# Kernel tuning notes

Measured on AMD Instinct MI355X. Metric: run time of the kernel, lower is better.

## Reference

```python
import jax, jax.numpy as jnp
import numpy as np

NUM_HEADS = 16
ATT_DIM = 1024
DEPTH = ATT_DIM // NUM_HEADS
LN_EPS = 1e-3  # keras LayerNormalization() default (hparams epsilon not passed through)


def setup_inputs() -> dict:
    key = jax.random.key(0)
    ks = jax.random.split(key, 16)
    B, S, D = 2, 2048, ATT_DIM
    s = 1.0 / np.sqrt(D)
    return {
        "query": jax.random.normal(ks[0], (B, S, D), jnp.float32),
        "key": jax.random.normal(ks[1], (B, S, D), jnp.float32),
        "value": jax.random.normal(ks[2], (B, S, D), jnp.float32),
        "Wq": jax.random.normal(ks[3], (D, ATT_DIM), jnp.float32) * s,
        "bq": jnp.zeros((ATT_DIM,), jnp.float32),
        "Wk": jax.random.normal(ks[4], (D, ATT_DIM), jnp.float32) * s,
        "bk": jnp.zeros((ATT_DIM,), jnp.float32),
        "Wv": jax.random.normal(ks[5], (D, ATT_DIM), jnp.float32) * s,
        "bv": jnp.zeros((ATT_DIM,), jnp.float32),
        "Wo": jax.random.normal(ks[6], (ATT_DIM, ATT_DIM), jnp.float32) * s,
        "bo": jnp.zeros((ATT_DIM,), jnp.float32),
        "gamma": jnp.ones((ATT_DIM,), jnp.float32),
        "beta": jnp.zeros((ATT_DIM,), jnp.float32),
    }


def _split_heads(x, B):
    # [B, S, D] -> [B, H, S, depth]
    return x.reshape(B, -1, NUM_HEADS, DEPTH).transpose(0, 2, 1, 3)


def reference(query, key, value, Wq, bq, Wk, bk, Wv, bv, Wo, bo, gamma, beta):
    B = query.shape[0]
    q = _split_heads(query @ Wq + bq, B)  # [B,H,Sq,d]
    k = _split_heads(key @ Wk + bk, B)    # [B,H,Sk,d]
    v = _split_heads(value @ Wv + bv, B)  # [B,H,Sk,d]
    scale = 1.0 / jnp.sqrt(jnp.asarray(DEPTH, q.dtype))
    logits = jnp.einsum('bhqd,bhkd->bhqk', q, k) * scale  # [B,H,Sq,Sk]
    attn = jax.nn.softmax(logits, axis=-1)
    ctx = jnp.einsum('bhqk,bhkd->bhqd', attn, v)  # [B,H,Sq,d]
    out = ctx.transpose(0, 2, 1, 3).reshape(B, -1, ATT_DIM)  # [B,Sq,D]
    out = out @ Wo + bo
    # LayerNorm over last dim (keras default epsilon=1e-3)
    mu = jnp.mean(out, axis=-1, keepdims=True)
    var = jnp.var(out, axis=-1, keepdims=True)
    out = (out - mu) * jax.lax.rsqrt(var + LN_EPS) * gamma + beta
    return out, attn
```

## Files before the change

### kernel.cpp

```cpp
#include <hip/hip_runtime.h>
#include <cstdint>
#include <cstddef>


#define S_LEN 2048
#define D_MODEL 1024
#define N_HEADS 16
#define DEPTH 64
#define BATCH 2
#define OUT0_ELEMS (BATCH * S_LEN * D_MODEL)

typedef __attribute__((ext_vector_type(8))) short short8;
typedef __attribute__((ext_vector_type(4))) short short4v;
typedef __attribute__((ext_vector_type(4))) float float4v;
typedef __attribute__((ext_vector_type(4))) uint16_t u16x4;

__device__ __forceinline__ float bf2f(uint16_t h) {
    uint32_t u = ((uint32_t)h) << 16;
    return __builtin_bit_cast(float, u);
}
__device__ __forceinline__ uint16_t f2bf(float f) {
    uint32_t u = __builtin_bit_cast(uint32_t, f);
    u += 0x7fffu + ((u >> 16) & 1u);
    return (uint16_t)(u >> 16);
}

__device__ __forceinline__ void async_load16(const void* g, void* l) {
    __builtin_amdgcn_global_load_lds(
        (const __attribute__((address_space(1))) void*)g,
        (__attribute__((address_space(3))) void*)l, 16, 0, 0);
}

template <typename Epi>
__device__ __forceinline__ void gemm_core_128x128(
    const uint16_t* __restrict__ A, const uint16_t* __restrict__ Bt,
    int K, Epi&& epi)
{
    __shared__ __align__(16) uint16_t la[128 * 32];
    __shared__ __align__(16) uint16_t lb[128 * 32];
    const int t = threadIdx.x;
    const int wave = t >> 6, lane = t & 63;
    const int quad = lane >> 4, lr = lane & 15;
    const int wm = (wave & 1) * 64, wn = (wave >> 1) * 64;
    const int row_a = t >> 2;
    const int kk = (t & 3) * 8;

    float4v acc[4][4] = {};

    for (int k0 = 0; k0 < K; k0 += 32) {
        async_load16(A  + (row_a      ) * K + k0 + kk, (char*)la + t * 16);
        async_load16(A  + (row_a + 64 ) * K + k0 + kk, (char*)la + 4096 + t * 16);
        async_load16(Bt + (row_a      ) * K + k0 + kk, (char*)lb + t * 16);
        async_load16(Bt + (row_a + 64 ) * K + k0 + kk, (char*)lb + 4096 + t * 16);
        __syncthreads();

        short8 af[4], bfr[4];
        #pragma unroll
        for (int i = 0; i < 4; i++)
            af[i] = *(const short8*)&la[(wm + i * 16 + lr) * 32 + quad * 8];
        #pragma unroll
        for (int j = 0; j < 4; j++)
            bfr[j] = *(const short8*)&lb[(wn + j * 16 + lr) * 32 + quad * 8];
        #pragma unroll
        for (int i = 0; i < 4; i++)
            #pragma unroll
            for (int j = 0; j < 4; j++)
                acc[i][j] = __builtin_amdgcn_mfma_f32_16x16x32_bf16(
                    af[i], bfr[j], acc[i][j], 0, 0, 0);
        __syncthreads();
    }

    #pragma unroll
    for (int i = 0; i < 4; i++)
        #pragma unroll
        for (int j = 0; j < 4; j++)
            #pragma unroll
            for (int r = 0; r < 4; r++)
                epi(wm + i * 16 + quad * 4 + r, wn + j * 16 + lr, acc[i][j][r]);
}

template <typename Epi>
__device__ __forceinline__ void gemm_split_128x128(
    const uint16_t* __restrict__ Ah, const uint16_t* __restrict__ Al,
    const uint16_t* __restrict__ Bh, const uint16_t* __restrict__ Bl,
    int K, Epi&& epi)
{
    __shared__ __align__(16) uint16_t lah[128 * 32];
    __shared__ __align__(16) uint16_t lal[128 * 32];
    __shared__ __align__(16) uint16_t lbh[128 * 32];
    __shared__ __align__(16) uint16_t lbl[128 * 32];
    const int t = threadIdx.x;
    const int wave = t >> 6, lane = t & 63;
    const int quad = lane >> 4, lr = lane & 15;
    const int wm = (wave & 1) * 64, wn = (wave >> 1) * 64;
    const int row_a = t >> 2;
    const int kk = (t & 3) * 8;

    float4v acc[4][4] = {};

    for (int k0 = 0; k0 < K; k0 += 32) {
        async_load16(Ah + (row_a     ) * K + k0 + kk, (char*)lah + t * 16);
        async_load16(Ah + (row_a + 64) * K + k0 + kk, (char*)lah + 4096 + t * 16);
        async_load16(Al + (row_a     ) * K + k0 + kk, (char*)lal + t * 16);
        async_load16(Al + (row_a + 64) * K + k0 + kk, (char*)lal + 4096 + t * 16);
        async_load16(Bh + (row_a     ) * K + k0 + kk, (char*)lbh + t * 16);
        async_load16(Bh + (row_a + 64) * K + k0 + kk, (char*)lbh + 4096 + t * 16);
        async_load16(Bl + (row_a     ) * K + k0 + kk, (char*)lbl + t * 16);
        async_load16(Bl + (row_a + 64) * K + k0 + kk, (char*)lbl + 4096 + t * 16);
        __syncthreads();

        short8 fah[4], fal[4], fbh[4], fbl[4];
        #pragma unroll
        for (int i = 0; i < 4; i++) {
            int off = (wm + i * 16 + lr) * 32 + quad * 8;
            fah[i] = *(const short8*)&lah[off];
            fal[i] = *(const short8*)&lal[off];
        }
        #pragma unroll
        for (int j = 0; j < 4; j++) {
            int off = (wn + j * 16 + lr) * 32 + quad * 8;
            fbh[j] = *(const short8*)&lbh[off];
            fbl[j] = *(const short8*)&lbl[off];
        }
        #pragma unroll
        for (int i = 0; i < 4; i++)
            #pragma unroll
            for (int j = 0; j < 4; j++) {
                acc[i][j] = __builtin_amdgcn_mfma_f32_16x16x32_bf16(
                    fah[i], fbh[j], acc[i][j], 0, 0, 0);
                acc[i][j] = __builtin_amdgcn_mfma_f32_16x16x32_bf16(
                    fah[i], fbl[j], acc[i][j], 0, 0, 0);
                acc[i][j] = __builtin_amdgcn_mfma_f32_16x16x32_bf16(
                    fal[i], fbh[j], acc[i][j], 0, 0, 0);
            }
        __syncthreads();
    }

    #pragma unroll
    for (int i = 0; i < 4; i++)
        #pragma unroll
        for (int j = 0; j < 4; j++)
            #pragma unroll
            for (int r = 0; r < 4; r++)
                epi(wm + i * 16 + quad * 4 + r, wn + j * 16 + lr, acc[i][j][r]);
}


__global__ __launch_bounds__(256) void prep_w_kernel(
    const float* __restrict__ wq, const float* __restrict__ wk,
    const float* __restrict__ wv, const float* __restrict__ wo,
    uint16_t* __restrict__ wqh, uint16_t* __restrict__ wql,
    uint16_t* __restrict__ wkh, uint16_t* __restrict__ wkl,
    uint16_t* __restrict__ wvt, uint16_t* __restrict__ wot)
{
    const int z = blockIdx.z;
    const float* src = z == 0 ? wq : z == 1 ? wk : z == 2 ? wv : wo;
    int idx = blockIdx.x * 256 + threadIdx.x;
    int n = idx >> 10, k = idx & 1023;
    float v = src[k * D_MODEL + n];
    uint16_t hi = f2bf(v);
    if (z == 0) { wqh[idx] = hi; wql[idx] = f2bf(v - bf2f(hi)); }
    else if (z == 1) { wkh[idx] = hi; wkl[idx] = f2bf(v - bf2f(hi)); }
    else if (z == 2) { wvt[idx] = hi; }
    else { wot[idx] = hi; }
}

__global__ __launch_bounds__(256) void split_x_kernel(
    const float* __restrict__ q, const float* __restrict__ k,
    const float* __restrict__ v,
    uint16_t* __restrict__ xqh, uint16_t* __restrict__ xql,
    uint16_t* __restrict__ xkh, uint16_t* __restrict__ xkl,
    uint16_t* __restrict__ xv)
{
    const int z = blockIdx.z;
    const float* src = z == 0 ? q : z == 1 ? k : v;
    int idx = (blockIdx.x * 256 + threadIdx.x) * 4;
    float4v f = *(const float4v*)(src + idx);
    u16x4 hi, lo;
    #pragma unroll
    for (int e = 0; e < 4; e++) {
        hi[e] = f2bf(f[e]);
        lo[e] = f2bf(f[e] - bf2f(hi[e]));
    }
    if (z == 0) { *(u16x4*)(xqh + idx) = hi; *(u16x4*)(xql + idx) = lo; }
    else if (z == 1) { *(u16x4*)(xkh + idx) = hi; *(u16x4*)(xkl + idx) = lo; }
    else { *(u16x4*)(xv + idx) = hi; }
}


__global__ __launch_bounds__(256) void qkproj_kernel(
    const uint16_t* __restrict__ xqh, const uint16_t* __restrict__ xql,
    const uint16_t* __restrict__ xkh, const uint16_t* __restrict__ xkl,
    const uint16_t* __restrict__ wqh, const uint16_t* __restrict__ wql,
    const uint16_t* __restrict__ wkh, const uint16_t* __restrict__ wkl,
    const float* __restrict__ bq, const float* __restrict__ bk,
    uint16_t* __restrict__ qh, uint16_t* __restrict__ ql,
    uint16_t* __restrict__ kh, uint16_t* __restrict__ kl)
{
    const int z = blockIdx.z;
    const uint16_t* Ah = (z == 0 ? xqh : xkh) + (size_t)blockIdx.y * 128 * D_MODEL;
    const uint16_t* Al = (z == 0 ? xql : xkl) + (size_t)blockIdx.y * 128 * D_MODEL;
    const uint16_t* Bh = (z == 0 ? wqh : wkh) + (size_t)blockIdx.x * 128 * D_MODEL;
    const uint16_t* Bl = (z == 0 ? wql : wkl) + (size_t)blockIdx.x * 128 * D_MODEL;
    const float* bias = z == 0 ? bq : bk;
    uint16_t* oh = z == 0 ? qh : kh;
    uint16_t* ol = z == 0 ? ql : kl;
    const int m0 = blockIdx.y * 128, n0 = blockIdx.x * 128;

    gemm_split_128x128(Ah, Al, Bh, Bl, D_MODEL, [&](int r, int c, float v) {
        int m = m0 + r, n = n0 + c;
        float val = v + bias[n];
        int b = m >> 11, s2 = m & 2047;
        int h = n >> 6, dp = n & 63;
        size_t o = (((size_t)(b * N_HEADS + h)) * S_LEN + s2) * DEPTH + dp;
        uint16_t hi = f2bf(val);
        oh[o] = hi;
        ol[o] = f2bf(val - bf2f(hi));
    });
}

__global__ __launch_bounds__(256) void vproj_kernel(
    const uint16_t* __restrict__ xv, const uint16_t* __restrict__ wvt,
    const float* __restrict__ bv, uint16_t* __restrict__ vt)
{
    const uint16_t* A  = xv + (size_t)blockIdx.y * 128 * D_MODEL;
    const uint16_t* Bt = wvt + (size_t)blockIdx.x * 128 * D_MODEL;
    const int m0 = blockIdx.y * 128, n0 = blockIdx.x * 128;

    gemm_core_128x128(A, Bt, D_MODEL, [&](int r, int c, float v) {
        int m = m0 + r, n = n0 + c;
        int b = m >> 11, s2 = m & 2047;
        int h = n >> 6, dp = n & 63;
        vt[(((size_t)(b * N_HEADS + h)) * DEPTH + dp) * S_LEN + s2] = f2bf(v + bv[n]);
    });
}

__global__ __launch_bounds__(512, 4) void attn_fused_kernel(
    const uint16_t* __restrict__ qh, const uint16_t* __restrict__ ql,
    const uint16_t* __restrict__ kh, const uint16_t* __restrict__ kl,
    const uint16_t* __restrict__ vt,
    float* __restrict__ attn, uint16_t* __restrict__ ctx)
{
    __shared__ __align__(16) uint16_t lkh[128 * 64];
    __shared__ __align__(16) uint16_t lkl[128 * 64];
    __shared__ __align__(16) uint16_t lvt[64 * 128];

    const int bh = blockIdx.y;
    const int b = bh >> 4, h = bh & 15;
    const int m0 = blockIdx.x * 128;
    const int t = threadIdx.x;
    const int wave = t >> 6, lane = t & 63;
    const int quad = lane >> 4, lr = lane & 15;
    const int q0 = m0 + wave * 16;
    const int mask = (lr & 7) << 4;

    const size_t qoff = ((size_t)bh * S_LEN + q0 + lr) * DEPTH + quad * 8;
    const short8 fqh0 = *(const short8*)&qh[qoff];
    const short8 fqh1 = *(const short8*)&qh[qoff + 32];
    const short8 fql0 = *(const short8*)&ql[qoff];
    const short8 fql1 = *(const short8*)&ql[qoff + 32];

    const uint16_t* khd = kh + (size_t)bh * S_LEN * DEPTH;
    const uint16_t* kld = kl + (size_t)bh * S_LEN * DEPTH;
    const uint16_t* vhd = vt + (size_t)bh * DEPTH * S_LEN;
    const int o1 = t * 16, o2 = 8192 + t * 16;
    const int kr1 = o1 >> 7, ke1 = ((o1 & 127) ^ ((kr1 & 7) << 4)) >> 1;
    const int kr2 = o2 >> 7, ke2 = ((o2 & 127) ^ ((kr2 & 7) << 4)) >> 1;
    const int vr1 = o1 >> 8, ve1 = ((o1 & 255) ^ ((vr1 & 7) << 4)) >> 1;
    const int vr2 = o2 >> 8, ve2 = ((o2 & 255) ^ ((vr2 & 7) << 4)) >> 1;

    float4v cacc[4] = {};
    float sum = 0.f;

    for (int kc = 0; kc < S_LEN; kc += 128) {
        async_load16(khd + (size_t)(kc + kr1) * DEPTH + ke1, (char*)lkh + o1);
        async_load16(khd + (size_t)(kc + kr2) * DEPTH + ke2, (char*)lkh + o2);
        async_load16(kld + (size_t)(kc + kr1) * DEPTH + ke1, (char*)lkl + o1);
        async_load16(kld + (size_t)(kc + kr2) * DEPTH + ke2, (char*)lkl + o2);
        async_load16(vhd + (size_t)vr1 * S_LEN + kc + ve1, (char*)lvt + o1);
        async_load16(vhd + (size_t)vr2 * S_LEN + kc + ve2, (char*)lvt + o2);
        __syncthreads();

        #pragma unroll
        for (int nt = 0; nt < 8; ++nt) {
            const int rowb = (nt * 16 + lr) * 128;
            const int cb0 = (quad * 16) ^ mask;
            short8 ah0 = *(const short8*)((const char*)lkh + rowb + cb0);
            short8 ah1 = *(const short8*)((const char*)lkh + rowb + (cb0 ^ 64));
            short8 al0 = *(const short8*)((const char*)lkl + rowb + cb0);
            short8 al1 = *(const short8*)((const char*)lkl + rowb + (cb0 ^ 64));
            float4v a = {0.f, 0.f, 0.f, 0.f};
            a = __builtin_amdgcn_mfma_f32_16x16x32_bf16(ah0, fqh0, a, 0, 0, 0);
            a = __builtin_amdgcn_mfma_f32_16x16x32_bf16(ah1, fqh1, a, 0, 0, 0);
            a = __builtin_amdgcn_mfma_f32_16x16x32_bf16(al0, fqh0, a, 0, 0, 0);
            a = __builtin_amdgcn_mfma_f32_16x16x32_bf16(al1, fqh1, a, 0, 0, 0);
            a = __builtin_amdgcn_mfma_f32_16x16x32_bf16(ah0, fql0, a, 0, 0, 0);
            a = __builtin_amdgcn_mfma_f32_16x16x32_bf16(ah1, fql1, a, 0, 0, 0);

            short4v pa;
            #pragma unroll
            for (int r = 0; r < 4; ++r) {
                float e = __expf(a[r] * 0.125f);
                sum += e;
                pa[r] = (short)f2bf(e);
            }
            #pragma unroll
            for (int dt = 0; dt < 4; ++dt) {
                const int vb = (dt * 16 + lr) * 256
                             + ((nt * 32 + quad * 8) ^ mask);
                short4v bv = *(const short4v*)((const char*)lvt + vb);
                cacc[dt] = __builtin_amdgcn_mfma_f32_16x16x16bf16_1k(
                    pa, bv, cacc[dt], 0, 0, 0);
            }
        }
        __syncthreads();
    }

    sum += __shfl_xor(sum, 16);
    sum += __shfl_xor(sum, 32);
    const float inv = 1.0f / sum;

    #pragma unroll
    for (int r = 0; r < 4; ++r) {
        const float invr = __shfl(inv, quad * 4 + r);
        #pragma unroll
        for (int dt = 0; dt < 4; ++dt) {
            ctx[((size_t)(b * S_LEN + q0 + quad * 4 + r)) * D_MODEL
                + h * DEPTH + dt * 16 + lr] = f2bf(cacc[dt][r] * invr);
        }
    }

    float* arow = attn + (size_t)bh * S_LEN * S_LEN + (size_t)(q0 + lr) * S_LEN;
    for (int kc = 0; kc < S_LEN; kc += 128) {
        async_load16(khd + (size_t)(kc + kr1) * DEPTH + ke1, (char*)lkh + o1);
        async_load16(khd + (size_t)(kc + kr2) * DEPTH + ke2, (char*)lkh + o2);
        async_load16(kld + (size_t)(kc + kr1) * DEPTH + ke1, (char*)lkl + o1);
        async_load16(kld + (size_t)(kc + kr2) * DEPTH + ke2, (char*)lkl + o2);
        __syncthreads();

        #pragma unroll
        for (int nt = 0; nt < 8; ++nt) {
            const int rowb = (nt * 16 + lr) * 128;
            const int cb0 = (quad * 16) ^ mask;
            short8 ah0 = *(const short8*)((const char*)lkh + rowb + cb0);
            short8 ah1 = *(const short8*)((const char*)lkh + rowb + (cb0 ^ 64));
            short8 al0 = *(const short8*)((const char*)lkl + rowb + cb0);
            short8 al1 = *(const short8*)((const char*)lkl + rowb + (cb0 ^ 64));
            float4v a = {0.f, 0.f, 0.f, 0.f};
            a = __builtin_amdgcn_mfma_f32_16x16x32_bf16(ah0, fqh0, a, 0, 0, 0);
            a = __builtin_amdgcn_mfma_f32_16x16x32_bf16(ah1, fqh1, a, 0, 0, 0);
            a = __builtin_amdgcn_mfma_f32_16x16x32_bf16(al0, fqh0, a, 0, 0, 0);
            a = __builtin_amdgcn_mfma_f32_16x16x32_bf16(al1, fqh1, a, 0, 0, 0);
            a = __builtin_amdgcn_mfma_f32_16x16x32_bf16(ah0, fql0, a, 0, 0, 0);
            a = __builtin_amdgcn_mfma_f32_16x16x32_bf16(ah1, fql1, a, 0, 0, 0);

            float4v p;
            #pragma unroll
            for (int r = 0; r < 4; ++r)
                p[r] = __expf(a[r] * 0.125f) * inv;
            *(float4v*)&arow[kc + nt * 16 + quad * 4] = p;
        }
        __syncthreads();
    }
}

__global__ __launch_bounds__(256) void proj_kernel(
    const uint16_t* __restrict__ ctx, const uint16_t* __restrict__ wot,
    const float* __restrict__ bo, float* __restrict__ pre)
{
    const uint16_t* A  = ctx + (size_t)blockIdx.y * 128 * D_MODEL;
    const uint16_t* Bt = wot + (size_t)blockIdx.x * 128 * D_MODEL;
    const int m0 = blockIdx.y * 128, n0 = blockIdx.x * 128;

    gemm_core_128x128(A, Bt, D_MODEL, [&](int r, int c, float v) {
        pre[(size_t)(m0 + r) * D_MODEL + (n0 + c)] = v + bo[n0 + c];
    });
}

__global__ __launch_bounds__(256) void ln_kernel(
    const float* __restrict__ pre, const float* __restrict__ gamma,
    const float* __restrict__ beta, float* __restrict__ out)
{
    const int t = threadIdx.x;
    const int row = blockIdx.x;
    const float4v x = *(const float4v*)(pre + (size_t)row * D_MODEL + t * 4);
    float s  = x[0] + x[1] + x[2] + x[3];
    float ss = x[0]*x[0] + x[1]*x[1] + x[2]*x[2] + x[3]*x[3];
    #pragma unroll
    for (int off = 32; off > 0; off >>= 1) {
        s  += __shfl_xor(s, off);
        ss += __shfl_xor(ss, off);
    }
    __shared__ float red[8];
    const int wave = t >> 6, lane = t & 63;
    if (lane == 0) { red[wave] = s; red[4 + wave] = ss; }
    __syncthreads();
    s  = (red[0] + red[1]) + (red[2] + red[3]);
    ss = (red[4] + red[5]) + (red[6] + red[7]);
    float mu  = s * (1.0f / 1024.0f);
    float var = ss * (1.0f / 1024.0f) - mu * mu;
    float inv = rsqrtf(var + 1e-3f);

    float4v g = *(const float4v*)(gamma + t * 4);
    float4v bb = *(const float4v*)(beta + t * 4);
    float4v o;
    #pragma unroll
    for (int j = 0; j < 4; j++)
        o[j] = (x[j] - mu) * inv * g[j] + bb[j];
    *(float4v*)(out + (size_t)row * D_MODEL + t * 4) = o;
}


extern "C" void kernel_launch(void* const* d_in, const int* in_sizes, int n_in,
                              void* d_out, int out_size, void* d_ws, size_t ws_size,
                              hipStream_t stream)
{
    const float* q_in = (const float*)d_in[0];
    const float* k_in = (const float*)d_in[1];
    const float* v_in = (const float*)d_in[2];
    const float* Wq   = (const float*)d_in[3];
    const float* bq   = (const float*)d_in[4];
    const float* Wk   = (const float*)d_in[5];
    const float* bk   = (const float*)d_in[6];
    const float* Wv   = (const float*)d_in[7];
    const float* bv   = (const float*)d_in[8];
    const float* Wo   = (const float*)d_in[9];
    const float* bo   = (const float*)d_in[10];
    const float* gamma= (const float*)d_in[11];
    const float* beta = (const float*)d_in[12];

    char* ws = (char*)d_ws;
    uint16_t* wqh = (uint16_t*)(ws);
    uint16_t* wql = (uint16_t*)(ws + (2u  << 20));
    uint16_t* wkh = (uint16_t*)(ws + (4u  << 20));
    uint16_t* wkl = (uint16_t*)(ws + (6u  << 20));
    uint16_t* wvt = (uint16_t*)(ws + (8u  << 20));
    uint16_t* wot = (uint16_t*)(ws + (10u << 20));
    uint16_t* xqh = (uint16_t*)(ws + (12u << 20));
    uint16_t* xql = (uint16_t*)(ws + (20u << 20));
    uint16_t* xkh = (uint16_t*)(ws + (28u << 20));
    uint16_t* xkl = (uint16_t*)(ws + (36u << 20));
    uint16_t* xv  = (uint16_t*)(ws + (44u << 20));
    uint16_t* qh  = (uint16_t*)(ws + (52u << 20));
    uint16_t* ql  = (uint16_t*)(ws + (60u << 20));
    uint16_t* kh  = (uint16_t*)(ws + (68u << 20));
    uint16_t* kl  = (uint16_t*)(ws + (76u << 20));
    uint16_t* vt  = (uint16_t*)(ws + (84u << 20));
    uint16_t* ctx = (uint16_t*)(ws + (92u << 20));
    float*    pre = (float*)   (ws + (100u << 20));

    float* out  = (float*)d_out;
    float* attn = out + OUT0_ELEMS;

    prep_w_kernel<<<dim3(4096, 1, 4), 256, 0, stream>>>(
        Wq, Wk, Wv, Wo, wqh, wql, wkh, wkl, wvt, wot);
    split_x_kernel<<<dim3(4096, 1, 3), 256, 0, stream>>>(
        q_in, k_in, v_in, xqh, xql, xkh, xkl, xv);
    qkproj_kernel<<<dim3(8, 32, 2), 256, 0, stream>>>(
        xqh, xql, xkh, xkl, wqh, wql, wkh, wkl, bq, bk, qh, ql, kh, kl);
    vproj_kernel<<<dim3(8, 32, 1), 256, 0, stream>>>(xv, wvt, bv, vt);
    attn_fused_kernel<<<dim3(16, 32), 512, 0, stream>>>(
        qh, ql, kh, kl, vt, attn, ctx);
    proj_kernel<<<dim3(8, 32, 1), 256, 0, stream>>>(ctx, wot, bo, pre);
    ln_kernel<<<dim3(4096), 256, 0, stream>>>(pre, gamma, beta, out);
}
```

Measured before the change: 866.9 us.

## Give attention waves 32 query rows and use bf16-only QK in the context pass

The attention kernel now runs 4 waves of 256 threads, each wave handling 32 query rows, so every K/V fragment read from LDS feeds two query tiles. The first pass, which builds the softmax sum and the context, drops the hi/lo split compensation and computes QK with bf16 high parts only, so K-low is no longer loaded there. The second pass, which writes the attention probabilities, keeps the split-precision QK. Weight prep now transposes through a shared-memory tile with coalesced vector loads and stores instead of strided scalar reads. Risks are more registers per wave and a softmax denominator from lower-precision logits that may not match the numerators written to attn.

```diff
diff --git a/kernel.cpp b/kernel.cpp
--- a/kernel.cpp
+++ b/kernel.cpp
@@ -155,14 +155,39 @@
 {
     const int z = blockIdx.z;
     const float* src = z == 0 ? wq : z == 1 ? wk : z == 2 ? wv : wo;
-    int idx = blockIdx.x * 256 + threadIdx.x;
-    int n = idx >> 10, k = idx & 1023;
-    float v = src[k * D_MODEL + n];
-    uint16_t hi = f2bf(v);
-    if (z == 0) { wqh[idx] = hi; wql[idx] = f2bf(v - bf2f(hi)); }
-    else if (z == 1) { wkh[idx] = hi; wkl[idx] = f2bf(v - bf2f(hi)); }
-    else if (z == 2) { wvt[idx] = hi; }
-    else { wot[idx] = hi; }
+    const int n0 = (blockIdx.x & 15) * 64;
+    const int k0 = (blockIdx.x >> 4) * 64;
+    __shared__ float lt[64][65];
+    const int t = threadIdx.x;
+    const int rr = t >> 4;
+    const int cc = (t & 15) * 4;
+
+    #pragma unroll
+    for (int p = 0; p < 4; ++p) {
+        const int row = rr + p * 16;
+        float4v f = *(const float4v*)&src[(size_t)(k0 + row) * D_MODEL + n0 + cc];
+        lt[row][cc + 0] = f[0]; lt[row][cc + 1] = f[1];
+        lt[row][cc + 2] = f[2]; lt[row][cc + 3] = f[3];
+    }
+    __syncthreads();
+
+    #pragma unroll
+    for (int p = 0; p < 4; ++p) {
+        const int n = rr + p * 16;
+        float v0 = lt[cc + 0][n], v1 = lt[cc + 1][n];
+        float v2 = lt[cc + 2][n], v3 = lt[cc + 3][n];
+        const int idx = (n0 + n) * D_MODEL + k0 + cc;
+        u16x4 hi, lo;
+        hi[0] = f2bf(v0); hi[1] = f2bf(v1); hi[2] = f2bf(v2); hi[3] = f2bf(v3);
+        if (z <= 1) {
+            lo[0] = f2bf(v0 - bf2f(hi[0])); lo[1] = f2bf(v1 - bf2f(hi[1]));
+            lo[2] = f2bf(v2 - bf2f(hi[2])); lo[3] = f2bf(v3 - bf2f(hi[3]));
+        }
+        if (z == 0)      { *(u16x4*)(wqh + idx) = hi; *(u16x4*)(wql + idx) = lo; }
+        else if (z == 1) { *(u16x4*)(wkh + idx) = hi; *(u16x4*)(wkl + idx) = lo; }
+        else if (z == 2) { *(u16x4*)(wvt + idx) = hi; }
+        else             { *(u16x4*)(wot + idx) = hi; }
+    }
 }
 
 __global__ __launch_bounds__(256) void split_x_kernel(
@@ -235,15 +260,14 @@
     });
 }
 
-__global__ __launch_bounds__(512, 4) void attn_fused_kernel(
+__global__ __launch_bounds__(256, 4) void attn_fused_kernel(
     const uint16_t* __restrict__ qh, const uint16_t* __restrict__ ql,
     const uint16_t* __restrict__ kh, const uint16_t* __restrict__ kl,
     const uint16_t* __restrict__ vt,
     float* __restrict__ attn, uint16_t* __restrict__ ctx)
 {
-    __shared__ __align__(16) uint16_t lkh[128 * 64];
-    __shared__ __align__(16) uint16_t lkl[128 * 64];
-    __shared__ __align__(16) uint16_t lvt[64 * 128];
+    __shared__ __align__(16) uint16_t lk[128 * 64];
+    __shared__ __align__(16) uint16_t lx[128 * 64];
 
     const int bh = blockIdx.y;
     const int b = bh >> 4, h = bh & 15;
@@ -251,114 +275,142 @@
     const int t = threadIdx.x;
     const int wave = t >> 6, lane = t & 63;
     const int quad = lane >> 4, lr = lane & 15;
-    const int q0 = m0 + wave * 16;
+    const int q0 = m0 + wave * 32;
     const int mask = (lr & 7) << 4;
 
-    const size_t qoff = ((size_t)bh * S_LEN + q0 + lr) * DEPTH + quad * 8;
-    const short8 fqh0 = *(const short8*)&qh[qoff];
-    const short8 fqh1 = *(const short8*)&qh[qoff + 32];
-    const short8 fql0 = *(const short8*)&ql[qoff];
-    const short8 fql1 = *(const short8*)&ql[qoff + 32];
+    const size_t qoffa = ((size_t)bh * S_LEN + q0 + lr) * DEPTH + quad * 8;
+    const size_t qoffb = qoffa + 16 * DEPTH;
+    const short8 fqh0a = *(const short8*)&qh[qoffa];
+    const short8 fqh1a = *(const short8*)&qh[qoffa + 32];
+    const short8 fqh0b = *(const short8*)&qh[qoffb];
+    const short8 fqh1b = *(const short8*)&qh[qoffb + 32];
 
     const uint16_t* khd = kh + (size_t)bh * S_LEN * DEPTH;
     const uint16_t* kld = kl + (size_t)bh * S_LEN * DEPTH;
     const uint16_t* vhd = vt + (size_t)bh * DEPTH * S_LEN;
-    const int o1 = t * 16, o2 = 8192 + t * 16;
-    const int kr1 = o1 >> 7, ke1 = ((o1 & 127) ^ ((kr1 & 7) << 4)) >> 1;
-    const int kr2 = o2 >> 7, ke2 = ((o2 & 127) ^ ((kr2 & 7) << 4)) >> 1;
-    const int vr1 = o1 >> 8, ve1 = ((o1 & 255) ^ ((vr1 & 7) << 4)) >> 1;
-    const int vr2 = o2 >> 8, ve2 = ((o2 & 255) ^ ((vr2 & 7) << 4)) >> 1;
-
-    float4v cacc[4] = {};
-    float sum = 0.f;
+
+    int kro[4], keo[4], vro[4], veo[4];
+    #pragma unroll
+    for (int j = 0; j < 4; ++j) {
+        const int o = t * 16 + j * 4096;
+        kro[j] = o >> 7; keo[j] = ((o & 127) ^ ((kro[j] & 7) << 4)) >> 1;
+        vro[j] = o >> 8; veo[j] = ((o & 255) ^ ((vro[j] & 7) << 4)) >> 1;
+    }
+
+    float4v cacca[4] = {}, caccb[4] = {};
+    float suma = 0.f, sumb = 0.f;
 
     for (int kc = 0; kc < S_LEN; kc += 128) {
-        async_load16(khd + (size_t)(kc + kr1) * DEPTH + ke1, (char*)lkh + o1);
-        async_load16(khd + (size_t)(kc + kr2) * DEPTH + ke2, (char*)lkh + o2);
-        async_load16(kld + (size_t)(kc + kr1) * DEPTH + ke1, (char*)lkl + o1);
-        async_load16(kld + (size_t)(kc + kr2) * DEPTH + ke2, (char*)lkl + o2);
-        async_load16(vhd + (size_t)vr1 * S_LEN + kc + ve1, (char*)lvt + o1);
-        async_load16(vhd + (size_t)vr2 * S_LEN + kc + ve2, (char*)lvt + o2);
+        #pragma unroll
+        for (int j = 0; j < 4; ++j) {
+            const int o = t * 16 + j * 4096;
+            async_load16(khd + (size_t)(kc + kro[j]) * DEPTH + keo[j], (char*)lk + o);
+            async_load16(vhd + (size_t)vro[j] * S_LEN + kc + veo[j], (char*)lx + o);
+        }
         __syncthreads();
 
         #pragma unroll
         for (int nt = 0; nt < 8; ++nt) {
             const int rowb = (nt * 16 + lr) * 128;
             const int cb0 = (quad * 16) ^ mask;
-            short8 ah0 = *(const short8*)((const char*)lkh + rowb + cb0);
-            short8 ah1 = *(const short8*)((const char*)lkh + rowb + (cb0 ^ 64));
-            short8 al0 = *(const short8*)((const char*)lkl + rowb + cb0);
-            short8 al1 = *(const short8*)((const char*)lkl + rowb + (cb0 ^ 64));
-            float4v a = {0.f, 0.f, 0.f, 0.f};
-            a = __builtin_amdgcn_mfma_f32_16x16x32_bf16(ah0, fqh0, a, 0, 0, 0);
-            a = __builtin_amdgcn_mfma_f32_16x16x32_bf16(ah1, fqh1, a, 0, 0, 0);
-            a = __builtin_amdgcn_mfma_f32_16x16x32_bf16(al0, fqh0, a, 0, 0, 0);
-            a = __builtin_amdgcn_mfma_f32_16x16x32_bf16(al1, fqh1, a, 0, 0, 0);
-            a = __builtin_amdgcn_mfma_f32_16x16x32_bf16(ah0, fql0, a, 0, 0, 0);
-            a = __builtin_amdgcn_mfma_f32_16x16x32_bf16(ah1, fql1, a, 0, 0, 0);
-
-            short4v pa;
+            short8 k0f = *(const short8*)((const char*)lk + rowb + cb0);
+            short8 k1f = *(const short8*)((const char*)lk + rowb + (cb0 ^ 64));
+            float4v aa = {0.f, 0.f, 0.f, 0.f};
+            float4v ab = {0.f, 0.f, 0.f, 0.f};
+            aa = __builtin_amdgcn_mfma_f32_16x16x32_bf16(k0f, fqh0a, aa, 0, 0, 0);
+            aa = __builtin_amdgcn_mfma_f32_16x16x32_bf16(k1f, fqh1a, aa, 0, 0, 0);
+            ab = __builtin_amdgcn_mfma_f32_16x16x32_bf16(k0f, fqh0b, ab, 0, 0, 0);
+            ab = __builtin_amdgcn_mfma_f32_16x16x32_bf16(k1f, fqh1b, ab, 0, 0, 0);
+
+            short4v paa, pab;
             #pragma unroll
             for (int r = 0; r < 4; ++r) {
-                float e = __expf(a[r] * 0.125f);
-                sum += e;
-                pa[r] = (short)f2bf(e);
+                float ea = __expf(aa[r] * 0.125f);
+                float eb = __expf(ab[r] * 0.125f);
+                suma += ea; sumb += eb;
+                paa[r] = (short)f2bf(ea);
+                pab[r] = (short)f2bf(eb);
             }
             #pragma unroll
             for (int dt = 0; dt < 4; ++dt) {
                 const int vb = (dt * 16 + lr) * 256
                              + ((nt * 32 + quad * 8) ^ mask);
-                short4v bv = *(const short4v*)((const char*)lvt + vb);
-                cacc[dt] = __builtin_amdgcn_mfma_f32_16x16x16bf16_1k(
-                    pa, bv, cacc[dt], 0, 0, 0);
+                short4v bv = *(const short4v*)((const char*)lx + vb);
+                cacca[dt] = __builtin_amdgcn_mfma_f32_16x16x16bf16_1k(
+                    paa, bv, cacca[dt], 0, 0, 0);
+                caccb[dt] = __builtin_amdgcn_mfma_f32_16x16x16bf16_1k(
+                    pab, bv, caccb[dt], 0, 0, 0);
             }
         }
         __syncthreads();
     }
 
-    sum += __shfl_xor(sum, 16);
-    sum += __shfl_xor(sum, 32);
-    const float inv = 1.0f / sum;
+    suma += __shfl_xor(suma, 16); suma += __shfl_xor(suma, 32);
+    sumb += __shfl_xor(sumb, 16); sumb += __shfl_xor(sumb, 32);
+    const float inva = 1.0f / suma;
+    const float invb = 1.0f / sumb;
 
     #pragma unroll
     for (int r = 0; r < 4; ++r) {
-        const float invr = __shfl(inv, quad * 4 + r);
+        const float ia = __shfl(inva, quad * 4 + r);
+        const float ib = __shfl(invb, quad * 4 + r);
         #pragma unroll
         for (int dt = 0; dt < 4; ++dt) {
-            ctx[((size_t)(b * S_LEN + q0 + quad * 4 + r)) * D_MODEL
-                + h * DEPTH + dt * 16 + lr] = f2bf(cacc[dt][r] * invr);
-        }
-    }
-
-    float* arow = attn + (size_t)bh * S_LEN * S_LEN + (size_t)(q0 + lr) * S_LEN;
+            const size_t cb = ((size_t)(b * S_LEN + q0 + quad * 4 + r)) * D_MODEL
+                            + h * DEPTH + dt * 16 + lr;
+            ctx[cb] = f2bf(cacca[dt][r] * ia);
+            ctx[cb + 16 * D_MODEL] = f2bf(caccb[dt][r] * ib);
+        }
+    }
+
+    const short8 fql0a = *(const short8*)&ql[qoffa];
+    const short8 fql1a = *(const short8*)&ql[qoffa + 32];
+    const short8 fql0b = *(const short8*)&ql[qoffb];
+    const short8 fql1b = *(const short8*)&ql[qoffb + 32];
+    float* arowa = attn + (size_t)bh * S_LEN * S_LEN + (size_t)(q0 + lr) * S_LEN;
+    float* arowb = arowa + 16 * S_LEN;
+
     for (int kc = 0; kc < S_LEN; kc += 128) {
-        async_load16(khd + (size_t)(kc + kr1) * DEPTH + ke1, (char*)lkh + o1);
-        async_load16(khd + (size_t)(kc + kr2) * DEPTH + ke2, (char*)lkh + o2);
-        async_load16(kld + (size_t)(kc + kr1) * DEPTH + ke1, (char*)lkl + o1);
-        async_load16(kld + (size_t)(kc + kr2) * DEPTH + ke2, (char*)lkl + o2);
+        #pragma unroll
+        for (int j = 0; j < 4; ++j) {
+            const int o = t * 16 + j * 4096;
+            async_load16(khd + (size_t)(kc + kro[j]) * DEPTH + keo[j], (char*)lk + o);
+            async_load16(kld + (size_t)(kc + kro[j]) * DEPTH + keo[j], (char*)lx + o);
+        }
         __syncthreads();
 
         #pragma unroll
         for (int nt = 0; nt < 8; ++nt) {
             const int rowb = (nt * 16 + lr) * 128;
             const int cb0 = (quad * 16) ^ mask;
-            short8 ah0 = *(const short8*)((const char*)lkh + rowb + cb0);
-            short8 ah1 = *(const short8*)((const char*)lkh + rowb + (cb0 ^ 64));
-            short8 al0 = *(const short8*)((const char*)lkl + rowb + cb0);
-            short8 al1 = *(const short8*)((const char*)lkl + rowb + (cb0 ^ 64));
-            float4v a = {0.f, 0.f, 0.f, 0.f};
-            a = __builtin_amdgcn_mfma_f32_16x16x32_bf16(ah0, fqh0, a, 0, 0, 0);
-            a = __builtin_amdgcn_mfma_f32_16x16x32_bf16(ah1, fqh1, a, 0, 0, 0);
-            a = __builtin_amdgcn_mfma_f32_16x16x32_bf16(al0, fqh0, a, 0, 0, 0);
-            a = __builtin_amdgcn_mfma_f32_16x16x32_bf16(al1, fqh1, a, 0, 0, 0);
-            a = __builtin_amdgcn_mfma_f32_16x16x32_bf16(ah0, fql0, a, 0, 0, 0);
-            a = __builtin_amdgcn_mfma_f32_16x16x32_bf16(ah1, fql1, a, 0, 0, 0);
-
-            float4v p;
-            #pragma unroll
-            for (int r = 0; r < 4; ++r)
-                p[r] = __expf(a[r] * 0.125f) * inv;
-            *(float4v*)&arow[kc + nt * 16 + quad * 4] = p;
+            short8 kh0 = *(const short8*)((const char*)lk + rowb + cb0);
+            short8 kh1 = *(const short8*)((const char*)lk + rowb + (cb0 ^ 64));
+            short8 kl0 = *(const short8*)((const char*)lx + rowb + cb0);
+            short8 kl1 = *(const short8*)((const char*)lx + rowb + (cb0 ^ 64));
+
+            float4v aa = {0.f, 0.f, 0.f, 0.f};
+            aa = __builtin_amdgcn_mfma_f32_16x16x32_bf16(kh0, fqh0a, aa, 0, 0, 0);
+            aa = __builtin_amdgcn_mfma_f32_16x16x32_bf16(kh1, fqh1a, aa, 0, 0, 0);
+            aa = __builtin_amdgcn_mfma_f32_16x16x32_bf16(kl0, fqh0a, aa, 0, 0, 0);
+            aa = __builtin_amdgcn_mfma_f32_16x16x32_bf16(kl1, fqh1a, aa, 0, 0, 0);
+            aa = __builtin_amdgcn_mfma_f32_16x16x32_bf16(kh0, fql0a, aa, 0, 0, 0);
+            aa = __builtin_amdgcn_mfma_f32_16x16x32_bf16(kh1, fql1a, aa, 0, 0, 0);
+            float4v ab = {0.f, 0.f, 0.f, 0.f};
+            ab = __builtin_amdgcn_mfma_f32_16x16x32_bf16(kh0, fqh0b, ab, 0, 0, 0);
+            ab = __builtin_amdgcn_mfma_f32_16x16x32_bf16(kh1, fqh1b, ab, 0, 0, 0);
+            ab = __builtin_amdgcn_mfma_f32_16x16x32_bf16(kl0, fqh0b, ab, 0, 0, 0);
+            ab = __builtin_amdgcn_mfma_f32_16x16x32_bf16(kl1, fqh1b, ab, 0, 0, 0);
+            ab = __builtin_amdgcn_mfma_f32_16x16x32_bf16(kh0, fql0b, ab, 0, 0, 0);
+            ab = __builtin_amdgcn_mfma_f32_16x16x32_bf16(kh1, fql1b, ab, 0, 0, 0);
+
+            float4v pa, pb;
+            #pragma unroll
+            for (int r = 0; r < 4; ++r) {
+                pa[r] = __expf(aa[r] * 0.125f) * inva;
+                pb[r] = __expf(ab[r] * 0.125f) * invb;
+            }
+            *(float4v*)&arowa[kc + nt * 16 + quad * 4] = pa;
+            *(float4v*)&arowb[kc + nt * 16 + quad * 4] = pb;
         }
         __syncthreads();
     }
@@ -452,14 +504,14 @@
     float* out  = (float*)d_out;
     float* attn = out + OUT0_ELEMS;
 
-    prep_w_kernel<<<dim3(4096, 1, 4), 256, 0, stream>>>(
+    prep_w_kernel<<<dim3(256, 1, 4), 256, 0, stream>>>(
         Wq, Wk, Wv, Wo, wqh, wql, wkh, wkl, wvt, wot);
     split_x_kernel<<<dim3(4096, 1, 3), 256, 0, stream>>>(
         q_in, k_in, v_in, xqh, xql, xkh, xkl, xv);
     qkproj_kernel<<<dim3(8, 32, 2), 256, 0, stream>>>(
         xqh, xql, xkh, xkl, wqh, wql, wkh, wkl, bq, bk, qh, ql, kh, kl);
     vproj_kernel<<<dim3(8, 32, 1), 256, 0, stream>>>(xv, wvt, bv, vt);
-    attn_fused_kernel<<<dim3(16, 32), 512, 0, stream>>>(
+    attn_fused_kernel<<<dim3(16, 32), 256, 0, stream>>>(
         qh, ql, kh, kl, vt, attn, ctx);
     proj_kernel<<<dim3(8, 32, 1), 256, 0, stream>>>(ctx, wot, bo, pre);
     ln_kernel<<<dim3(4096), 256, 0, stream>>>(pre, gamma, beta, out);
```

Measured after the change: 855.1 us. About the same (-1.4%).
